# Performance work log

Hardware: AMD Instinct MI355X
Metric: run time of the kernel (lower is better)

Reference implementation:

```python
import jax, jax.numpy as jnp
import numpy as np

# ---- constants from init_kwargs ----
RES = 128                       # config.grid.resolution (base_resolution, n_levels=1)
LOG2_T = 22
TABLE_SIZE = 1 << LOG2_T        # hashmap entries
N_G = 4                         # features per level, gaussian grid
N_V = 8                         # features per level, vmf grid
BB_MIN = jnp.array([-10.0, -10.0, -10.0], dtype=jnp.float32)
BB_MAX = jnp.array([10.0, 10.0, 10.0], dtype=jnp.float32)
N_PTS = 1048576

_P2 = np.uint32(2654435761)
_P3 = np.uint32(805459861)
# 8 trilinear corner offsets [8,3]
_CORNERS = jnp.array([[i, j, k] for i in (0, 1) for j in (0, 1) for k in (0, 1)], dtype=jnp.int32)


def hashgrid_lookup(table, pos):
    """tcnn-style HashGrid (1 level, trilinear). pos: [N,3] in [0,1] domain."""
    x = pos * RES                     # scale to grid coords
    x0 = jnp.floor(x)
    w = x - x0                        # [N,3] trilinear weights
    corners = x0.astype(jnp.int32)[:, None, :] + _CORNERS[None]   # [N,8,3]
    cu = corners.astype(jnp.uint32)
    h = (cu[..., 0] ^ (cu[..., 1] * _P2) ^ (cu[..., 2] * _P3)) & jnp.uint32(TABLE_SIZE - 1)
    feat = table[h.astype(jnp.int32)]                              # [N,8,F] gather
    wts = jnp.prod(jnp.where(_CORNERS[None].astype(bool), w[:, None, :], 1.0 - w[:, None, :]), axis=-1)  # [N,8]
    return jnp.einsum('nc,ncf->nf', wts, feat)                     # [N,F]


def sample_vpls(pos, gauss_table, vmf_table):
    """Accumulate encodings over the 27-neighbor stencil (accumulate_gaussians=True)."""
    block = 1.0 / RES
    npos = (pos - BB_MIN) / (BB_MAX - BB_MIN)      # normalized [N,3]
    total_g = jnp.zeros((pos.shape[0], N_G), dtype=jnp.float32)
    total_v = jnp.zeros((pos.shape[0], N_V), dtype=jnp.float32)
    for dx in (-1, 0, 1):
        for dy in (-1, 0, 1):
            for dz in (-1, 0, 1):
                off = jnp.array([dx, dy, dz], dtype=jnp.float32) * block
                p = npos + off
                total_g = total_g + hashgrid_lookup(gauss_table, p)
                total_v = total_v + hashgrid_lookup(vmf_table, p)
    return total_g, total_v


def encode(gaussians, vmf):
    # gaussian_mean_encoding='sigmoid' (non-raw -> rescale to bbox)
    mean = jax.nn.sigmoid(gaussians[:, :3]) * (BB_MAX - BB_MIN) + BB_MIN
    variance = jax.nn.softplus(gaussians[:, 3])[:, None]          # 'softplus'
    sharpness = jnp.exp(vmf[:, 0])[:, None]                        # 'exp'
    ax = vmf[:, 1:4]                                               # 'normalize' (F.normalize, eps=1e-12)
    axis = ax / jnp.maximum(jnp.linalg.norm(ax, axis=1, keepdims=True), 1e-12)
    amplitude = jax.nn.sigmoid(vmf[:, 4:7])                        # 'sigmoid'
    g_out = jnp.concatenate([mean, variance], axis=1)             # [N,4]
    v_out = jnp.concatenate([sharpness, axis, amplitude], axis=1) # [N,7]
    return g_out, v_out


def setup_inputs() -> dict:
    key = jax.random.key(0)
    k1, k2, k3 = jax.random.split(key, 3)
    # world-space query positions inside the bounding box
    u = jax.random.uniform(k1, (N_PTS, 3), dtype=jnp.float32)
    pos = u * (BB_MAX - BB_MIN) + BB_MIN
    # hash-grid feature tables (tcnn initializes near zero)
    gauss_table = jax.random.normal(k2, (TABLE_SIZE, N_G), dtype=jnp.float32) * 0.1
    vmf_table = jax.random.normal(k3, (TABLE_SIZE, N_V), dtype=jnp.float32) * 0.1
    return {"pos": pos, "gauss_table": gauss_table, "vmf_table": vmf_table}


def reference(pos, gauss_table, vmf_table):
    gaussians, vmf = sample_vpls(pos, gauss_table, vmf_table)
    return encode(gaussians, vmf)
```

## Files before the change

### kernel.cpp

```cpp
#include <hip/hip_runtime.h>
#include <hip/hip_fp16.h>
#include <cstdint>

#define TABLE_MASK 0x3FFFFFu
#define P2 2654435761u
#define P3 805459861u

#define XD 128
#define YD 132
#define ZD 132
#define RECU 12
#define NB3 (128 * 128 * 8)
#define SCAN_BLKS (NB3 / 1024)
#define BUILD_BLKS (131 * 66)

__device__ __forceinline__ float sigmoidf_(float x) { return 1.0f / (1.0f + expf(-x)); }

__device__ __forceinline__ uint32_t f2h2(float a, float b) {
    __half2 h = __floats2half2_rn(a, b);
    return *reinterpret_cast<uint32_t*>(&h);
}
__device__ __forceinline__ __half2 u2h2(uint32_t u) {
    return *reinterpret_cast<__half2*>(&u);
}

__device__ __forceinline__ int bin_key3(float px, float py, float pz)
{
    float x = ((px + 10.0f) / 20.0f) * 128.0f;
    float y = ((py + 10.0f) / 20.0f) * 128.0f;
    float z = ((pz + 10.0f) / 20.0f) * 128.0f;
    int ix = min(max((int)floorf(x), 0), 127);
    int iy = min(max((int)floorf(y), 0), 127);
    int iz = min(max((int)floorf(z), 0), 127);
    return (((iz << 7) + iy) << 3) + (ix >> 4);
}

__global__ __launch_bounds__(256)
void build_hist_kernel(const float4* __restrict__ gauss,
                       const float4* __restrict__ vmf,
                       uint32_t* __restrict__ exdx,
                       const float* __restrict__ pos,
                       uint32_t* __restrict__ hist, int n)
{
    if (blockIdx.x >= BUILD_BLKS) {
        int p = (blockIdx.x - BUILD_BLKS) * blockDim.x + threadIdx.x;
        if (p < n) {
            int k = bin_key3(pos[3 * p], pos[3 * p + 1], pos[3 * p + 2]);
            atomicAdd(&hist[k], 1u);
        }
        return;
    }

    __shared__ float sm[2][131][13];
    int bidx = blockIdx.x;
    int yp = bidx % 66;
    int rz = 1 + bidx / 66;
    int ry0 = 1 + 2 * yp;
    int t = threadIdx.x;

    for (int l = t; l < 262; l += 256) {
        int row = (l >= 131) ? 1 : 0;
        int cell = l - row * 131;
        int ry = ry0 + row;
        if (ry <= 131) {
            int xc = 1 + cell;
            uint32_t ux = (uint32_t)(xc - 2);
            uint32_t uy = (uint32_t)(ry - 2);
            uint32_t uz = (uint32_t)(rz - 2);
            uint32_t h = (ux ^ (uy * P2) ^ (uz * P3)) & TABLE_MASK;
            float4 g  = gauss[h];
            float4 v0 = vmf[(size_t)2 * h];
            float4 v1 = vmf[(size_t)2 * h + 1];
            float* s = sm[row][cell];
            s[0] = g.x;  s[1] = g.y;  s[2]  = g.z;  s[3]  = g.w;
            s[4] = v0.x; s[5] = v0.y; s[6]  = v0.z; s[7]  = v0.w;
            s[8] = v1.x; s[9] = v1.y; s[10] = v1.z; s[11] = v1.w;
        }
    }
    __syncthreads();

    int row = t >> 7;
    int c   = t & 127;
    int ry  = ry0 + row;
    if (ry > 131) return;

    uint32_t rec[12];
#pragma unroll
    for (int m = 0; m < 6; ++m) {
        float e0 = sm[row][c][2*m]   + sm[row][c+1][2*m]   + sm[row][c+2][2*m];
        float e1 = sm[row][c][2*m+1] + sm[row][c+1][2*m+1] + sm[row][c+2][2*m+1];
        float d0 = sm[row][c+3][2*m]   - sm[row][c][2*m];
        float d1 = sm[row][c+3][2*m+1] - sm[row][c][2*m+1];
        rec[m]     = f2h2(e0, e1);
        rec[6 + m] = f2h2(d0, d1);
    }
    size_t o = (((size_t)rz * YD + (size_t)ry) * XD + (size_t)c) * RECU;
    *(uint4*)(exdx + o)     = make_uint4(rec[0], rec[1], rec[2],  rec[3]);
    *(uint4*)(exdx + o + 4) = make_uint4(rec[4], rec[5], rec[6],  rec[7]);
    *(uint4*)(exdx + o + 8) = make_uint4(rec[8], rec[9], rec[10], rec[11]);
}

__global__ __launch_bounds__(1024)
void scanA_kernel(const uint32_t* __restrict__ hist,
                  uint32_t* __restrict__ cursor,
                  uint32_t* __restrict__ sums)
{
    __shared__ uint32_t buf[1024];
    int t = threadIdx.x;
    int base = blockIdx.x * 1024;
    uint32_t v = hist[base + t];
    buf[t] = v;
    __syncthreads();
    for (int off = 1; off < 1024; off <<= 1) {
        uint32_t x = (t >= off) ? buf[t - off] : 0u;
        __syncthreads();
        buf[t] += x;
        __syncthreads();
    }
    cursor[base + t] = buf[t] - v;
    if (t == 1023) sums[blockIdx.x] = buf[t];
}

__global__ __launch_bounds__(256)
void scatter_kernel(const float* __restrict__ pos,
                    uint32_t* __restrict__ cursor,
                    const uint32_t* __restrict__ sums,
                    float4* __restrict__ sortedPts, int n)
{
    __shared__ uint32_t soff[SCAN_BLKS];
    int t = threadIdx.x;
    if (t < SCAN_BLKS) soff[t] = sums[t];
    __syncthreads();
    for (int off = 1; off < SCAN_BLKS; off <<= 1) {
        uint32_t v = 0;
        if (t < SCAN_BLKS && t >= off) v = soff[t - off];
        __syncthreads();
        if (t < SCAN_BLKS) soff[t] += v;
        __syncthreads();
    }

    int p = blockIdx.x * blockDim.x + t;
    if (p >= n) return;
    float px = pos[3 * p], py = pos[3 * p + 1], pz = pos[3 * p + 2];
    int k = bin_key3(px, py, pz);
    int chunk = k >> 10;
    uint32_t base = (chunk > 0) ? soff[chunk - 1] : 0u;
    uint32_t slot = base + atomicAdd(&cursor[k], 1u);
    sortedPts[slot] = make_float4(px, py, pz, __uint_as_float((uint32_t)p));
}

__device__ __forceinline__ void consume_cell(const uint4& A, const uint4& B, const uint4& C,
                                             __half2 wxh, float w, float* acc)
{
    uint32_t e[6] = {A.x, A.y, A.z, A.w, B.x, B.y};
    uint32_t d[6] = {B.z, B.w, C.x, C.y, C.z, C.w};
#pragma unroll
    for (int m = 0; m < 6; ++m) {
        __half2 v = __hfma2(wxh, u2h2(d[m]), u2h2(e[m]));
        float2 f = __half22float2(v);
        acc[2*m]     = fmaf(w, f.x, acc[2*m]);
        acc[2*m + 1] = fmaf(w, f.y, acc[2*m + 1]);
    }
}

__global__ __launch_bounds__(256, 2)
void vapl_grid_sorted_kernel(const float4* __restrict__ sortedPts,
                             const uint32_t* __restrict__ exdx,
                             float* __restrict__ out,
                             int n)
{
    int bid = blockIdx.x;
    int nb  = gridDim.x;
    int b2  = ((nb & 7) == 0) ? ((bid & 7) * (nb >> 3) + (bid >> 3)) : bid;
    int s = b2 * (int)blockDim.x + (int)threadIdx.x;
    if (s >= n) return;

    float4 pt = sortedPts[s];
    int p = (int)__float_as_uint(pt.w);

    float x = ((pt.x + 10.0f) / 20.0f) * 128.0f;
    float y = ((pt.y + 10.0f) / 20.0f) * 128.0f;
    float z = ((pt.z + 10.0f) / 20.0f) * 128.0f;

    float fx = floorf(x), fy = floorf(y), fz = floorf(z);
    int ix = (int)fx, iy = (int)fy, iz = (int)fz;
    float wx = x - fx, wy = y - fy, wz = z - fz;

    float ay[4] = {1.0f - wy, 1.0f, 1.0f, wy};
    float az[4] = {1.0f - wz, 1.0f, 1.0f, wz};
    __half2 wxh = __float2half2_rn(wx);

    int bx = ix + 1, by = iy + 1, bz = iz + 1;

    uint32_t idx16[16];
    float    w16[16];
#pragma unroll
    for (int k = 0; k < 4; ++k) {
#pragma unroll
        for (int j = 0; j < 4; ++j) {
            idx16[k*4 + j] = (((uint32_t)(bz + k) * YD + (uint32_t)(by + j)) * XD
                              + (uint32_t)(bx - 1)) * RECU;
            w16[k*4 + j] = ay[j] * az[k];
        }
    }

    float acc[12] = {0.f,0.f,0.f,0.f,0.f,0.f,0.f,0.f,0.f,0.f,0.f,0.f};

    uint4 A[8][3], B[8][3];
#pragma unroll
    for (int c = 0; c < 8; ++c) {
        const uint32_t* r = exdx + idx16[c];
        A[c][0] = *(const uint4*)(r);
        A[c][1] = *(const uint4*)(r + 4);
        A[c][2] = *(const uint4*)(r + 8);
    }
#pragma unroll
    for (int c = 0; c < 8; ++c) {
        const uint32_t* r = exdx + idx16[8 + c];
        B[c][0] = *(const uint4*)(r);
        B[c][1] = *(const uint4*)(r + 4);
        B[c][2] = *(const uint4*)(r + 8);
    }
#pragma unroll
    for (int c = 0; c < 8; ++c)
        consume_cell(A[c][0], A[c][1], A[c][2], wxh, w16[c], acc);
#pragma unroll
    for (int c = 0; c < 8; ++c)
        consume_cell(B[c][0], B[c][1], B[c][2], wxh, w16[8 + c], acc);

    float m0 = sigmoidf_(acc[0]) * 20.0f - 10.0f;
    float m1 = sigmoidf_(acc[1]) * 20.0f - 10.0f;
    float m2 = sigmoidf_(acc[2]) * 20.0f - 10.0f;
    float var = fmaxf(acc[3], 0.0f) + log1pf(expf(-fabsf(acc[3])));

    float sharp = expf(acc[4]);
    float nrm = fmaxf(sqrtf(acc[5]*acc[5] + acc[6]*acc[6] + acc[7]*acc[7]), 1e-12f);
    float a0 = acc[5] / nrm, a1 = acc[6] / nrm, a2 = acc[7] / nrm;
    float amp0 = sigmoidf_(acc[8]);
    float amp1 = sigmoidf_(acc[9]);
    float amp2 = sigmoidf_(acc[10]);

    float* og = out + (size_t)p * 4;
    *(float4*)og = make_float4(m0, m1, m2, var);

    float* ov = out + (size_t)n * 4 + (size_t)p * 7;
    ov[0] = sharp;
    ov[1] = a0;
    ov[2] = a1;
    ov[3] = a2;
    ov[4] = amp0;
    ov[5] = amp1;
    ov[6] = amp2;
}

__global__ __launch_bounds__(256)
void vapl_grid_kernel(const float* __restrict__ pos,
                      const float4* __restrict__ gauss,
                      const float4* __restrict__ vmf,
                      float* __restrict__ out,
                      int n)
{
    int p = blockIdx.x * blockDim.x + threadIdx.x;
    if (p >= n) return;

    float px = pos[3 * p + 0];
    float py = pos[3 * p + 1];
    float pz = pos[3 * p + 2];

    float x = ((px + 10.0f) / 20.0f) * 128.0f;
    float y = ((py + 10.0f) / 20.0f) * 128.0f;
    float z = ((pz + 10.0f) / 20.0f) * 128.0f;

    float fx = floorf(x), fy = floorf(y), fz = floorf(z);
    int ix = (int)fx, iy = (int)fy, iz = (int)fz;
    float wx = x - fx, wy = y - fy, wz = z - fz;

    float ax[4] = {1.0f - wx, 1.0f, 1.0f, wx};
    float ay[4] = {1.0f - wy, 1.0f, 1.0f, wy};
    float az[4] = {1.0f - wz, 1.0f, 1.0f, wz};

    uint32_t hx[4], hy[4], hz[4];
#pragma unroll
    for (int i = 0; i < 4; ++i) {
        hx[i] = (uint32_t)(ix - 1 + i);
        hy[i] = (uint32_t)(iy - 1 + i) * P2;
        hz[i] = (uint32_t)(iz - 1 + i) * P3;
    }

    float tg0 = 0.f, tg1 = 0.f, tg2 = 0.f, tg3 = 0.f;
    float tv0 = 0.f, tv1 = 0.f, tv2 = 0.f, tv3 = 0.f;
    float tv4 = 0.f, tv5 = 0.f, tv6 = 0.f, tv7 = 0.f;

    for (int k = 0; k < 4; ++k) {
        for (int j = 0; j < 4; ++j) {
            uint32_t hyz = hy[j] ^ hz[k];
            float wyz = ay[j] * az[k];
#pragma unroll
            for (int i = 0; i < 4; ++i) {
                uint32_t h = (hx[i] ^ hyz) & TABLE_MASK;
                float w = ax[i] * wyz;
                float4 g  = gauss[h];
                float4 v0 = vmf[(size_t)2 * h];
                float4 v1 = vmf[(size_t)2 * h + 1];
                tg0 = fmaf(w, g.x,  tg0);
                tg1 = fmaf(w, g.y,  tg1);
                tg2 = fmaf(w, g.z,  tg2);
                tg3 = fmaf(w, g.w,  tg3);
                tv0 = fmaf(w, v0.x, tv0);
                tv1 = fmaf(w, v0.y, tv1);
                tv2 = fmaf(w, v0.z, tv2);
                tv3 = fmaf(w, v0.w, tv3);
                tv4 = fmaf(w, v1.x, tv4);
                tv5 = fmaf(w, v1.y, tv5);
                tv6 = fmaf(w, v1.z, tv6);
                tv7 = fmaf(w, v1.w, tv7);
            }
        }
    }

    float m0 = sigmoidf_(tg0) * 20.0f - 10.0f;
    float m1 = sigmoidf_(tg1) * 20.0f - 10.0f;
    float m2 = sigmoidf_(tg2) * 20.0f - 10.0f;
    float var = fmaxf(tg3, 0.0f) + log1pf(expf(-fabsf(tg3)));

    float sharp = expf(tv0);
    float nrm = fmaxf(sqrtf(tv1 * tv1 + tv2 * tv2 + tv3 * tv3), 1e-12f);
    float a0 = tv1 / nrm, a1 = tv2 / nrm, a2 = tv3 / nrm;
    float amp0 = sigmoidf_(tv4);
    float amp1 = sigmoidf_(tv5);
    float amp2 = sigmoidf_(tv6);

    float* og = out + (size_t)p * 4;
    og[0] = m0;
    og[1] = m1;
    og[2] = m2;
    og[3] = var;

    float* ov = out + (size_t)n * 4 + (size_t)p * 7;
    ov[0] = sharp;
    ov[1] = a0;
    ov[2] = a1;
    ov[3] = a2;
    ov[4] = amp0;
    ov[5] = amp1;
    ov[6] = amp2;
}

extern "C" void kernel_launch(void* const* d_in, const int* in_sizes, int n_in,
                              void* d_out, int out_size, void* d_ws, size_t ws_size,
                              hipStream_t stream) {
    const float*  pos   = (const float*)d_in[0];
    const float4* gauss = (const float4*)d_in[1];
    const float4* vmf   = (const float4*)d_in[2];
    float* out = (float*)d_out;
    int n = in_sizes[0] / 3;

    size_t off = 0;
    char* ws = (char*)d_ws;
    uint32_t* exdx   = (uint32_t*)(ws + off);  off += (size_t)XD * YD * ZD * RECU * 4;
    off = (off + 255) & ~(size_t)255;
    uint32_t* hist   = (uint32_t*)(ws + off);  off += (size_t)NB3 * 4;
    uint32_t* cursor = (uint32_t*)(ws + off);  off += (size_t)NB3 * 4;
    uint32_t* sums   = (uint32_t*)(ws + off);  off += 256 * 4;
    off = (off + 255) & ~(size_t)255;
    float4* sortedPts = (float4*)(ws + off);   off += (size_t)n * 16;
    const size_t need = off;

    dim3 block(256);
    dim3 grid((n + 255) / 256);

    if (ws_size >= need) {
        hipMemsetAsync(hist, 0, (size_t)NB3 * 4, stream);
        hipLaunchKernelGGL(build_hist_kernel, dim3(BUILD_BLKS + 4096), block, 0, stream,
                           gauss, vmf, exdx, pos, hist, n);
        hipLaunchKernelGGL(scanA_kernel, dim3(SCAN_BLKS), dim3(1024), 0, stream, hist, cursor, sums);
        hipLaunchKernelGGL(scatter_kernel, grid, block, 0, stream, pos, cursor, sums, sortedPts, n);
        hipLaunchKernelGGL(vapl_grid_sorted_kernel, grid, block, 0, stream,
                           sortedPts, exdx, out, n);
    } else {
        hipLaunchKernelGGL(vapl_grid_kernel, grid, block, 0, stream, pos, gauss, vmf, out, n);
    }
}
```

Before: 260.5 us.

## Pad grid records to 64 bytes, interleave ex/dx, pipeline cell loads, nontemporal I/O

```diff
diff --git a/kernel.cpp b/kernel.cpp
--- a/kernel.cpp
+++ b/kernel.cpp
@@ -9,10 +9,13 @@
 #define XD 128
 #define YD 132
 #define ZD 132
-#define RECU 12
+#define RECU 16
 #define NB3 (128 * 128 * 8)
 #define SCAN_BLKS (NB3 / 1024)
 #define BUILD_BLKS (131 * 66)
+
+typedef unsigned int uint4v __attribute__((ext_vector_type(4)));
+typedef float float4v __attribute__((ext_vector_type(4)));
 
 __device__ __forceinline__ float sigmoidf_(float x) { return 1.0f / (1.0f + expf(-x)); }
 
@@ -84,20 +87,25 @@
     int ry  = ry0 + row;
     if (ry > 131) return;
 
-    uint32_t rec[12];
+    uint32_t ex[6], dx[6];
 #pragma unroll
     for (int m = 0; m < 6; ++m) {
         float e0 = sm[row][c][2*m]   + sm[row][c+1][2*m]   + sm[row][c+2][2*m];
         float e1 = sm[row][c][2*m+1] + sm[row][c+1][2*m+1] + sm[row][c+2][2*m+1];
         float d0 = sm[row][c+3][2*m]   - sm[row][c][2*m];
         float d1 = sm[row][c+3][2*m+1] - sm[row][c][2*m+1];
-        rec[m]     = f2h2(e0, e1);
-        rec[6 + m] = f2h2(d0, d1);
+        ex[m] = f2h2(e0, e1);
+        dx[m] = f2h2(d0, d1);
     }
     size_t o = (((size_t)rz * YD + (size_t)ry) * XD + (size_t)c) * RECU;
-    *(uint4*)(exdx + o)     = make_uint4(rec[0], rec[1], rec[2],  rec[3]);
-    *(uint4*)(exdx + o + 4) = make_uint4(rec[4], rec[5], rec[6],  rec[7]);
-    *(uint4*)(exdx + o + 8) = make_uint4(rec[8], rec[9], rec[10], rec[11]);
+    uint4v w0 = {ex[0], dx[0], ex[1], dx[1]};
+    uint4v w1 = {ex[2], dx[2], ex[3], dx[3]};
+    uint4v w2 = {ex[4], dx[4], ex[5], dx[5]};
+    uint4v w3 = {0u, 0u, 0u, 0u};
+    __builtin_nontemporal_store(w0, (uint4v*)(exdx + o));
+    __builtin_nontemporal_store(w1, (uint4v*)(exdx + o + 4));
+    __builtin_nontemporal_store(w2, (uint4v*)(exdx + o + 8));
+    __builtin_nontemporal_store(w3, (uint4v*)(exdx + o + 12));
 }
 
 __global__ __launch_bounds__(1024)
@@ -149,18 +157,22 @@
     sortedPts[slot] = make_float4(px, py, pz, __uint_as_float((uint32_t)p));
 }
 
-__device__ __forceinline__ void consume_cell(const uint4& A, const uint4& B, const uint4& C,
+__device__ __forceinline__ void consume_cell(const uint4v& v0, const uint4v& v1, const uint4v& v2,
                                              __half2 wxh, float w, float* acc)
 {
-    uint32_t e[6] = {A.x, A.y, A.z, A.w, B.x, B.y};
-    uint32_t d[6] = {B.z, B.w, C.x, C.y, C.z, C.w};
-#pragma unroll
-    for (int m = 0; m < 6; ++m) {
-        __half2 v = __hfma2(wxh, u2h2(d[m]), u2h2(e[m]));
-        float2 f = __half22float2(v);
-        acc[2*m]     = fmaf(w, f.x, acc[2*m]);
-        acc[2*m + 1] = fmaf(w, f.y, acc[2*m + 1]);
-    }
+    __half2 t; float2 f;
+    t = __hfma2(wxh, u2h2(v0.y), u2h2(v0.x)); f = __half22float2(t);
+    acc[0] = fmaf(w, f.x, acc[0]); acc[1] = fmaf(w, f.y, acc[1]);
+    t = __hfma2(wxh, u2h2(v0.w), u2h2(v0.z)); f = __half22float2(t);
+    acc[2] = fmaf(w, f.x, acc[2]); acc[3] = fmaf(w, f.y, acc[3]);
+    t = __hfma2(wxh, u2h2(v1.y), u2h2(v1.x)); f = __half22float2(t);
+    acc[4] = fmaf(w, f.x, acc[4]); acc[5] = fmaf(w, f.y, acc[5]);
+    t = __hfma2(wxh, u2h2(v1.w), u2h2(v1.z)); f = __half22float2(t);
+    acc[6] = fmaf(w, f.x, acc[6]); acc[7] = fmaf(w, f.y, acc[7]);
+    t = __hfma2(wxh, u2h2(v2.y), u2h2(v2.x)); f = __half22float2(t);
+    acc[8] = fmaf(w, f.x, acc[8]); acc[9] = fmaf(w, f.y, acc[9]);
+    t = __hfma2(wxh, u2h2(v2.w), u2h2(v2.z)); f = __half22float2(t);
+    acc[10] = fmaf(w, f.x, acc[10]); acc[11] = fmaf(w, f.y, acc[11]);
 }
 
 __global__ __launch_bounds__(256, 2)
@@ -175,7 +187,7 @@
     int s = b2 * (int)blockDim.x + (int)threadIdx.x;
     if (s >= n) return;
 
-    float4 pt = sortedPts[s];
+    float4v pt = __builtin_nontemporal_load((const float4v*)(sortedPts + s));
     int p = (int)__float_as_uint(pt.w);
 
     float x = ((pt.x + 10.0f) / 20.0f) * 128.0f;
@@ -206,27 +218,34 @@
 
     float acc[12] = {0.f,0.f,0.f,0.f,0.f,0.f,0.f,0.f,0.f,0.f,0.f,0.f};
 
-    uint4 A[8][3], B[8][3];
-#pragma unroll
-    for (int c = 0; c < 8; ++c) {
+    uint4v buf[2][4][3];
+#pragma unroll
+    for (int c = 0; c < 4; ++c) {
         const uint32_t* r = exdx + idx16[c];
-        A[c][0] = *(const uint4*)(r);
-        A[c][1] = *(const uint4*)(r + 4);
-        A[c][2] = *(const uint4*)(r + 8);
-    }
-#pragma unroll
-    for (int c = 0; c < 8; ++c) {
-        const uint32_t* r = exdx + idx16[8 + c];
-        B[c][0] = *(const uint4*)(r);
-        B[c][1] = *(const uint4*)(r + 4);
-        B[c][2] = *(const uint4*)(r + 8);
-    }
-#pragma unroll
-    for (int c = 0; c < 8; ++c)
-        consume_cell(A[c][0], A[c][1], A[c][2], wxh, w16[c], acc);
-#pragma unroll
-    for (int c = 0; c < 8; ++c)
-        consume_cell(B[c][0], B[c][1], B[c][2], wxh, w16[8 + c], acc);
+        buf[0][c][0] = *(const uint4v*)(r);
+        buf[0][c][1] = *(const uint4v*)(r + 4);
+        buf[0][c][2] = *(const uint4v*)(r + 8);
+    }
+    __builtin_amdgcn_sched_barrier(0);
+#pragma unroll
+    for (int b = 0; b < 4; ++b) {
+        const int cur = b & 1, nxt = cur ^ 1;
+        if (b < 3) {
+#pragma unroll
+            for (int c = 0; c < 4; ++c) {
+                const uint32_t* r = exdx + idx16[(b + 1) * 4 + c];
+                buf[nxt][c][0] = *(const uint4v*)(r);
+                buf[nxt][c][1] = *(const uint4v*)(r + 4);
+                buf[nxt][c][2] = *(const uint4v*)(r + 8);
+            }
+            __builtin_amdgcn_sched_barrier(0);
+        }
+#pragma unroll
+        for (int c = 0; c < 4; ++c)
+            consume_cell(buf[cur][c][0], buf[cur][c][1], buf[cur][c][2],
+                         wxh, w16[b*4 + c], acc);
+        __builtin_amdgcn_sched_barrier(0);
+    }
 
     float m0 = sigmoidf_(acc[0]) * 20.0f - 10.0f;
     float m1 = sigmoidf_(acc[1]) * 20.0f - 10.0f;
@@ -240,17 +259,17 @@
     float amp1 = sigmoidf_(acc[9]);
     float amp2 = sigmoidf_(acc[10]);
 
-    float* og = out + (size_t)p * 4;
-    *(float4*)og = make_float4(m0, m1, m2, var);
+    float4v og = {m0, m1, m2, var};
+    __builtin_nontemporal_store(og, (float4v*)(out + (size_t)p * 4));
 
     float* ov = out + (size_t)n * 4 + (size_t)p * 7;
-    ov[0] = sharp;
-    ov[1] = a0;
-    ov[2] = a1;
-    ov[3] = a2;
-    ov[4] = amp0;
-    ov[5] = amp1;
-    ov[6] = amp2;
+    __builtin_nontemporal_store(sharp, ov + 0);
+    __builtin_nontemporal_store(a0,    ov + 1);
+    __builtin_nontemporal_store(a1,    ov + 2);
+    __builtin_nontemporal_store(a2,    ov + 3);
+    __builtin_nontemporal_store(amp0,  ov + 4);
+    __builtin_nontemporal_store(amp1,  ov + 5);
+    __builtin_nontemporal_store(amp2,  ov + 6);
 }
 
 __global__ __launch_bounds__(256)
@@ -370,7 +389,7 @@
     dim3 grid((n + 255) / 256);
 
     if (ws_size >= need) {
-        hipMemsetAsync(hist, 0, (size_t)NB3 * 4, stream);
+        (void)hipMemsetAsync(hist, 0, (size_t)NB3 * 4, stream);
         hipLaunchKernelGGL(build_hist_kernel, dim3(BUILD_BLKS + 4096), block, 0, stream,
                            gauss, vmf, exdx, pos, hist, n);
         hipLaunchKernelGGL(scanA_kernel, dim3(SCAN_BLKS), dim3(1024), 0, stream, hist, cursor, sums);
```

New measurement: 358.6 us. +37.7%, slower.
